# Kernel optimization log

Hardware: AMD Instinct MI355X
Metric: run time of the kernel (lower is better)

The kernel has to match this reference:

```python
import jax, jax.numpy as jnp
import numpy as np

B, T, D = 4, 2048, 256
KQ, V, H = 16, 16, 8
SCALE = float(np.sqrt(KQ))


def _lin(key, din, dout):
    k1, k2 = jax.random.split(key)
    lim = 1.0 / np.sqrt(din)
    w = jax.random.uniform(k1, (din, dout), minval=-lim, maxval=lim, dtype=jnp.float32)
    b = jax.random.uniform(k2, (dout,), minval=-lim, maxval=lim, dtype=jnp.float32)
    return w, b


def setup_inputs() -> dict:
    key = jax.random.key(0)
    ks = jax.random.split(key, 14)
    x = jax.random.normal(ks[0], (B, 3, T), dtype=jnp.float32)
    h = jax.random.normal(ks[1], (B, D, T), dtype=jnp.float32)
    q_w1, q_b1 = _lin(ks[2], D, KQ * H)
    q_w2, q_b2 = _lin(ks[3], KQ * H, KQ * H)
    k_w1, k_b1 = _lin(ks[4], D, KQ * H)
    k_w2, k_b2 = _lin(ks[5], KQ * H, KQ * H)
    v_w1, v_b1 = _lin(ks[6], D, V * H)
    v_w2, v_b2 = _lin(ks[7], V * H, V * H)
    xm_w1, xm_b1 = _lin(ks[8], V * H, V * H)
    xm_w2, xm_b2 = _lin(ks[9], V * H, H)
    ho_w, ho_b = _lin(ks[10], V * H, D)
    # GVP: Wh [v_in, dim_h], Wu [dim_h, v_out]; torch init = randn
    gvp_Wh = jax.random.normal(ks[11], (H, H), dtype=jnp.float32)
    gvp_Wu = jax.random.normal(ks[12], (H, 1), dtype=jnp.float32)
    return dict(x=x, h=h,
                q_w1=q_w1, q_b1=q_b1, q_w2=q_w2, q_b2=q_b2,
                k_w1=k_w1, k_b1=k_b1, k_w2=k_w2, k_b2=k_b2,
                v_w1=v_w1, v_b1=v_b1, v_w2=v_w2, v_b2=v_b2,
                xm_w1=xm_w1, xm_b1=xm_b1, xm_w2=xm_w2, xm_b2=xm_b2,
                ho_w=ho_w, ho_b=ho_b, gvp_Wh=gvp_Wh, gvp_Wu=gvp_Wu)


def _mlp(x, w1, b1, w2, b2):
    return jax.nn.silu(x @ w1 + b1) @ w2 + b2


def _rotate_half(t):
    # interleaved pairs (x1,x2) -> (-x2, x1), lucidrains rotary convention
    t2 = t.reshape(t.shape[:-1] + (t.shape[-1] // 2, 2))
    a, b = t2[..., 0], t2[..., 1]
    return jnp.stack((-b, a), axis=-1).reshape(t.shape)


def _rope(t):
    # t: [B, H, T, KQ]
    seq = t.shape[-2]
    inv = 1.0 / (10000.0 ** (jnp.arange(0, KQ, 2, dtype=jnp.float32) / KQ))
    f = jnp.arange(seq, dtype=jnp.float32)[:, None] * inv[None, :]   # [T, KQ/2]
    f = jnp.repeat(f, 2, axis=-1)                                    # [T, KQ]
    return t * jnp.cos(f) + _rotate_half(t) * jnp.sin(f)


def _forward(x, h,
             q_w1, q_b1, q_w2, q_b2,
             k_w1, k_b1, k_w2, k_b2,
             v_w1, v_b1, v_w2, v_b2,
             xm_w1, xm_b1, xm_w2, xm_b2,
             ho_w, ho_b, gvp_Wh, gvp_Wu):
    b, _, t = x.shape
    h_m = jnp.transpose(h, (0, 2, 1)).reshape(b * t, D)     # merge_time_dim
    q = _mlp(h_m, q_w1, q_b1, q_w2, q_b2)                   # [B*T, KQ*H]
    k = _mlp(h_m, k_w1, k_b1, k_w2, k_b2)
    v = _mlp(h_m, v_w1, v_b1, v_w2, v_b2)                   # [B*T, V*H]
    v_x = _mlp(v, xm_w1, xm_b1, xm_w2, xm_b2)               # [B*T, H]

    q = q.reshape(b, t, H, KQ).transpose(0, 2, 1, 3)        # [B,H,T,KQ]
    k = k.reshape(b, t, H, KQ).transpose(0, 2, 1, 3)
    v4 = v.reshape(b, t, H, V).transpose(0, 2, 1, 3)        # [B,H,T,V]
    v_x = v_x.reshape(b, t, H).transpose(0, 2, 1)           # [B,H,T]

    q = _rope(q)
    k = _rope(k)

    attn = jax.nn.softmax(
        jnp.einsum('bhtd,bhsd->bhts', q, k) / SCALE, axis=-1)  # [B,H,T,T]

    h_upd = jnp.einsum('bhts,bhsd->bhtd', attn, v4)         # [B,H,T,V]
    h_upd = h_upd.transpose(0, 2, 1, 3).reshape(b, t, H * V)
    h_upd = (h_upd @ ho_w + ho_b).transpose(0, 2, 1)        # [B,D,T]
    h_out = h + h_upd

    attn_w = attn * v_x[:, :, None, :]                      # weight key axis s
    gamma = attn_w.sum(axis=-1)                             # [B,H,T]
    weighted_x = jnp.einsum('bhij,bdj->bhdi', attn_w, x)    # [B,H,3,T]
    x_head = gamma[:, :, None, :] * x[:, None, :, :] - weighted_x  # [B,H,3,T]
    x_upd = x_head.transpose(0, 3, 1, 2).reshape(b * t, H, 3)      # [B*T,H,3]

    # GVP vector branch (scalar branch does not affect returned vectors)
    Vh = jnp.einsum('bvc,vh->bhc', x_upd, gvp_Wh)           # [B*T,H,3]
    Vu = jnp.einsum('bhc,hu->buc', Vh, gvp_Wu)              # [B*T,1,3]
    gate = jnp.linalg.norm(Vu, axis=-1, keepdims=True)      # [B*T,1,1]
    delta = jax.nn.sigmoid(gate) * Vu                       # [B*T,1,3]
    delta = delta[:, 0, :].reshape(b, t, 3).transpose(0, 2, 1)  # separate_time_dim -> [B,3,T]
    x_out = x + delta
    return x_out, h_out


def reference(x, h,
              q_w1, q_b1, q_w2, q_b2,
              k_w1, k_b1, k_w2, k_b2,
              v_w1, v_b1, v_w2, v_b2,
              xm_w1, xm_b1, xm_w2, xm_b2,
              ho_w, ho_b, gvp_Wh, gvp_Wu):
    return _forward(x, h,
                    q_w1, q_b1, q_w2, q_b2,
                    k_w1, k_b1, k_w2, k_b2,
                    v_w1, v_b1, v_w2, v_b2,
                    xm_w1, xm_b1, xm_w2, xm_b2,
                    ho_w, ho_b, gvp_Wh, gvp_Wu)
```

## Files before the change

kernel.cpp:

```cpp
#include <hip/hip_runtime.h>
#include <hip/hip_bf16.h>
#include <math.h>

typedef __attribute__((ext_vector_type(8))) short s16x8;
typedef __attribute__((ext_vector_type(4))) float f32x4;

__device__ __forceinline__ float silu(float a) {
    return a / (1.f + __expf(-a));
}
__device__ __forceinline__ unsigned short f2b(float f) {
    __hip_bfloat16 h = __float2bfloat16(f);
    return *reinterpret_cast<unsigned short*>(&h);
}

__global__ __launch_bounds__(256) void wprep(
    const float* __restrict__ qw1, const float* __restrict__ kw1,
    const float* __restrict__ vw1, const float* __restrict__ qw2,
    const float* __restrict__ kw2, const float* __restrict__ vw2,
    const float* __restrict__ xmw1, const float* __restrict__ xmw2,
    unsigned short* __restrict__ w1T, unsigned short* __restrict__ w2T,
    unsigned short* __restrict__ xm1T, unsigned short* __restrict__ xm2T)
{
    int idx = blockIdx.x * 256 + threadIdx.x;
    if (idx < 98304) {
        int m = idx >> 15, r = idx & 32767;
        int n = r >> 8, k = r & 255;
        const float* src = (m == 0) ? qw1 : (m == 1) ? kw1 : vw1;
        w1T[idx] = f2b(src[k * 128 + n]);
    } else if (idx < 147456) {
        int r0 = idx - 98304;
        int m = r0 >> 14, r = r0 & 16383;
        int n = r >> 7, k = r & 127;
        const float* src = (m == 0) ? qw2 : (m == 1) ? kw2 : vw2;
        w2T[r0] = f2b(src[k * 128 + n]);
    } else if (idx < 163840) {
        int r = idx - 147456;
        int n = r >> 7, k = r & 127;
        xm1T[r] = f2b(xmw1[k * 128 + n]);
    } else if (idx < 165888) {
        int r = idx - 163840;
        int n = r >> 7, k = r & 127;
        xm2T[r] = (n < 8) ? f2b(xmw2[k * 8 + n]) : (unsigned short)0;
    }
}

__global__ __launch_bounds__(256) void qkv_mfma(
    const float* __restrict__ x, const float* __restrict__ h,
    const float* __restrict__ qb1, const float* __restrict__ qb2,
    const float* __restrict__ kb1, const float* __restrict__ kb2,
    const float* __restrict__ vb1, const float* __restrict__ vb2,
    const float* __restrict__ xmb1, const float* __restrict__ xmb2,
    const unsigned short* __restrict__ w1T, const unsigned short* __restrict__ w2T,
    const unsigned short* __restrict__ xm1T, const unsigned short* __restrict__ xm2T,
    unsigned short* __restrict__ q_bf, unsigned short* __restrict__ k_bf,
    unsigned short* __restrict__ vT_bf)
{
    const int blk = blockIdx.x;
    const int b   = blk >> 7;
    const int t0  = (blk & 127) << 4;
    const int tid = threadIdx.x;
    const int nq   = tid >> 6;
    const int lane = tid & 63;
    const int m_   = lane & 15;
    const int quad = lane >> 4;

    __shared__ __align__(16) unsigned short hA[16][264];
    __shared__ __align__(16) unsigned short hidA[16][136];
    __shared__ __align__(16) unsigned short voutA[16][136];
    __shared__ float vxs[16][8];

    #pragma unroll
    for (int g = 0; g < 4; g++) {
        float4 hv = *(const float4*)(h + ((size_t)(b * 256 + tid)) * 2048
                                       + t0 + g * 4);
        hA[g * 4 + 0][tid] = f2b(hv.x);
        hA[g * 4 + 1][tid] = f2b(hv.y);
        hA[g * 4 + 2][tid] = f2b(hv.z);
        hA[g * 4 + 3][tid] = f2b(hv.w);
    }
    __syncthreads();

    auto gemm1 = [&](const unsigned short* w1m, const float* b1) {
        f32x4 acc[2] = {{0.f,0.f,0.f,0.f},{0.f,0.f,0.f,0.f}};
        #pragma unroll
        for (int kc = 0; kc < 8; kc++) {
            s16x8 af = *(const s16x8*)&hA[m_][kc * 32 + quad * 8];
            #pragma unroll
            for (int nt = 0; nt < 2; nt++) {
                const s16x8 bf = *(const s16x8*)(w1m
                    + (size_t)(nq * 32 + nt * 16 + m_) * 256 + kc * 32 + quad * 8);
                acc[nt] = __builtin_amdgcn_mfma_f32_16x16x32_bf16(
                    af, bf, acc[nt], 0, 0, 0);
            }
        }
        #pragma unroll
        for (int nt = 0; nt < 2; nt++) {
            int col = nq * 32 + nt * 16 + m_;
            float bia = b1[col];
            #pragma unroll
            for (int i = 0; i < 4; i++)
                hidA[quad * 4 + i][col] = f2b(silu(acc[nt][i] + bia));
        }
    };
    auto gemm2 = [&](const unsigned short* w2m, f32x4 acc[2]) {
        #pragma unroll
        for (int kc = 0; kc < 4; kc++) {
            s16x8 af = *(const s16x8*)&hidA[m_][kc * 32 + quad * 8];
            #pragma unroll
            for (int nt = 0; nt < 2; nt++) {
                const s16x8 bf = *(const s16x8*)(w2m
                    + (size_t)(nq * 32 + nt * 16 + m_) * 128 + kc * 32 + quad * 8);
                acc[nt] = __builtin_amdgcn_mfma_f32_16x16x32_bf16(
                    af, bf, acc[nt], 0, 0, 0);
            }
        }
    };
    auto rope_store = [&](f32x4 acc[2], const float* b2,
                          unsigned short* dst, float scale) {
        #pragma unroll
        for (int nt = 0; nt < 2; nt++) {
            int col  = nq * 32 + nt * 16 + m_;
            int head = col >> 4, dim = col & 15;
            float inv = exp2f(-(float)(dim >> 1) * 0.125f * 13.28771238f);
            float bia = b2[col];
            #pragma unroll
            for (int i = 0; i < 4; i++) {
                int t = t0 + quad * 4 + i;
                float a  = acc[nt][i] + bia;
                float pr = __shfl_xor(a, 1);
                float f  = (float)t * inv;
                float cs = cosf(f), sn = sinf(f);
                float o  = (dim & 1) ? (a * cs + pr * sn) : (a * cs - pr * sn);
                dst[((size_t)(b * 8 + head) * 2048 + t) * 16 + dim] =
                    f2b(o * scale);
            }
        }
    };

    gemm1(w1T, qb1);
    __syncthreads();
    {
        f32x4 acc[2] = {{0.f,0.f,0.f,0.f},{0.f,0.f,0.f,0.f}};
        gemm2(w2T, acc);
        rope_store(acc, qb2, q_bf, 0.25f);
    }
    __syncthreads();

    gemm1(w1T + 32768, kb1);
    __syncthreads();
    {
        f32x4 acc[2] = {{0.f,0.f,0.f,0.f},{0.f,0.f,0.f,0.f}};
        gemm2(w2T + 16384, acc);
        rope_store(acc, kb2, k_bf, 1.0f);
    }
    __syncthreads();

    gemm1(w1T + 65536, vb1);
    __syncthreads();
    {
        f32x4 acc[2] = {{0.f,0.f,0.f,0.f},{0.f,0.f,0.f,0.f}};
        gemm2(w2T + 32768, acc);
        #pragma unroll
        for (int nt = 0; nt < 2; nt++) {
            int col = nq * 32 + nt * 16 + m_;
            float bia = vb2[col];
            #pragma unroll
            for (int i = 0; i < 4; i++)
                voutA[quad * 4 + i][col] = f2b(acc[nt][i] + bia);
        }
    }
    __syncthreads();

    {
        int col = tid >> 1, tg = tid & 1;
        s16x8 pk;
        #pragma unroll
        for (int e = 0; e < 8; e++)
            pk[e] = (short)voutA[tg * 8 + e][col];
        *(s16x8*)(vT_bf + ((size_t)(b * 8 + (col >> 4)) * 32 + (col & 15)) * 2048
                        + t0 + tg * 8) = pk;
    }
    {
        f32x4 acc[2] = {{0.f,0.f,0.f,0.f},{0.f,0.f,0.f,0.f}};
        #pragma unroll
        for (int kc = 0; kc < 4; kc++) {
            s16x8 af = *(const s16x8*)&voutA[m_][kc * 32 + quad * 8];
            #pragma unroll
            for (int nt = 0; nt < 2; nt++) {
                const s16x8 bf = *(const s16x8*)(xm1T
                    + (size_t)(nq * 32 + nt * 16 + m_) * 128 + kc * 32 + quad * 8);
                acc[nt] = __builtin_amdgcn_mfma_f32_16x16x32_bf16(
                    af, bf, acc[nt], 0, 0, 0);
            }
        }
        __syncthreads();
        #pragma unroll
        for (int nt = 0; nt < 2; nt++) {
            int col = nq * 32 + nt * 16 + m_;
            float bia = xmb1[col];
            #pragma unroll
            for (int i = 0; i < 4; i++)
                hidA[quad * 4 + i][col] = f2b(silu(acc[nt][i] + bia));
        }
    }
    __syncthreads();

    if (nq == 0) {
        f32x4 a2 = {0.f, 0.f, 0.f, 0.f};
        #pragma unroll
        for (int kc = 0; kc < 4; kc++) {
            s16x8 af = *(const s16x8*)&hidA[m_][kc * 32 + quad * 8];
            const s16x8 bf = *(const s16x8*)(xm2T
                + (size_t)m_ * 128 + kc * 32 + quad * 8);
            a2 = __builtin_amdgcn_mfma_f32_16x16x32_bf16(af, bf, a2, 0, 0, 0);
        }
        if (m_ < 8) {
            float bia = xmb2[m_];
            #pragma unroll
            for (int i = 0; i < 4; i++)
                vxs[quad * 4 + i][m_] = a2[i] + bia;
        }
    }
    __syncthreads();

    #pragma unroll
    for (int r = 0; r < 2; r++) {
        int i  = tid + r * 256;
        int hh = i >> 6, c = (i >> 4) & 3, tt = i & 15;
        float val = vxs[tt][hh];
        if (c)
            val *= x[((size_t)(b * 3 + (c - 1))) * 2048 + t0 + tt];
        vT_bf[((size_t)(b * 8 + hh) * 32 + 16 + c) * 2048 + t0 + tt] = f2b(val);
    }
    if (tid < 192) {
        int hh = tid / 24, rem = tid % 24;
        int c  = 20 + (rem >> 1), tg = rem & 1;
        s16x8 z = {0,0,0,0,0,0,0,0};
        *(s16x8*)(vT_bf + ((size_t)(b * 8 + hh) * 32 + c) * 2048
                        + t0 + tg * 8) = z;
    }
}

__global__ __launch_bounds__(64) void attn_mfma(
    const unsigned short* __restrict__ q_bf,
    const unsigned short* __restrict__ k_bf,
    const unsigned short* __restrict__ vT_bf,
    float* __restrict__ opart)
{
    const int blk  = blockIdx.x;
    const int sp   = blk >> 10;
    const int bh   = (blk >> 5) & 31;
    const int qs   = (blk & 31) << 6;
    const int lane = threadIdx.x;
    const int m_   = lane & 15;
    const int quad = lane >> 4;

    __shared__ __align__(16) unsigned short Elds[4][2][16 * 72];

    const s16x8 zs = {0, 0, 0, 0, 0, 0, 0, 0};
    const f32x4 zero = {0.f, 0.f, 0.f, 0.f};

    s16x8 qfrag[4];
    #pragma unroll
    for (int qt = 0; qt < 4; qt++) {
        qfrag[qt] = zs;
        if (quad < 2)
            qfrag[qt] = *(const s16x8*)(q_bf +
                ((size_t)(bh * 2048 + qs + qt * 16 + m_) * 16 + quad * 8));
    }

    f32x4 O0[4], O1[4];
    float lsq[4];
    #pragma unroll
    for (int qt = 0; qt < 4; qt++) {
        O0[qt] = zero; O1[qt] = zero; lsq[qt] = 0.f;
    }

    const unsigned short* kb = k_bf + ((size_t)bh * 2048 + sp * 1024) * 16;
    const unsigned short* vb = vT_bf + (size_t)bh * 32 * 2048 + sp * 1024;

    for (int kt = 0; kt < 16; kt++) {
        const int k0 = kt * 64;
        const int buf = kt & 1;

        s16x8 kf[4];
        #pragma unroll
        for (int n = 0; n < 4; n++) {
            kf[n] = zs;
            if (quad < 2)
                kf[n] = *(const s16x8*)(kb +
                      ((size_t)(k0 + n * 16 + m_) * 16 + quad * 8));
        }
        s16x8 vf0[2], vf1[2];
        #pragma unroll
        for (int c = 0; c < 2; c++) {
            vf0[c] = *(const s16x8*)(vb + (size_t)m_ * 2048
                                        + k0 + c * 32 + quad * 8);
            vf1[c] = *(const s16x8*)(vb + (size_t)(16 + m_) * 2048
                                        + k0 + c * 32 + quad * 8);
        }

        #pragma unroll
        for (int qt = 0; qt < 4; qt++) {
            #pragma unroll
            for (int n = 0; n < 4; n++) {
                f32x4 E = __builtin_amdgcn_mfma_f32_16x16x32_bf16(
                    kf[n], qfrag[qt], zero, 0, 0, 0);
                float e0 = __expf(E[0]);
                float e1 = __expf(E[1]);
                float e2 = __expf(E[2]);
                float e3 = __expf(E[3]);
                lsq[qt] += e0 + e1 + e2 + e3;
                uint2 pk;
                pk.x = (unsigned)f2b(e0) | ((unsigned)f2b(e1) << 16);
                pk.y = (unsigned)f2b(e2) | ((unsigned)f2b(e3) << 16);
                *(uint2*)&Elds[qt][buf][m_ * 72 + n * 16 + quad * 4] = pk;
            }
        }
        __builtin_amdgcn_s_waitcnt(0xc07f);

        #pragma unroll
        for (int qt = 0; qt < 4; qt++) {
            #pragma unroll
            for (int c = 0; c < 2; c++) {
                s16x8 af = *(const s16x8*)
                    &Elds[qt][buf][m_ * 72 + c * 32 + quad * 8];
                O0[qt] = __builtin_amdgcn_mfma_f32_16x16x32_bf16(
                    af, vf0[c], O0[qt], 0, 0, 0);
                O1[qt] = __builtin_amdgcn_mfma_f32_16x16x32_bf16(
                    af, vf1[c], O1[qt], 0, 0, 0);
            }
        }
    }

    #pragma unroll
    for (int qt = 0; qt < 4; qt++) {
        float s = lsq[qt];
        s += __shfl_xor(s, 16);
        s += __shfl_xor(s, 32);
        float* opb = opart + ((size_t)(sp * 32 + bh) * 2048 + qs + qt * 16) * 24;
        #pragma unroll
        for (int i = 0; i < 4; i++) {
            int row = quad * 4 + i;
            float* ob = opb + row * 24;
            ob[m_] = O0[qt][i];
            if (m_ < 4) ob[16 + m_] = O1[qt][i];
        }
        if (quad == 0) opb[m_ * 24 + 20] = s;
    }
}

__global__ __launch_bounds__(256) void epi_kernel(
    const float* __restrict__ opart,
    const float* __restrict__ x, const float* __restrict__ hin,
    const float* __restrict__ how, const float* __restrict__ hob,
    const float* __restrict__ Wh, const float* __restrict__ Wu,
    float* __restrict__ out)
{
    const int blk = blockIdx.x;
    const int b  = blk >> 8;
    const int t0 = (blk & 255) << 3;
    const int tid = threadIdx.x;
    const size_t half = (size_t)32 * 2048 * 24;

    __shared__ __align__(16) float hv[128][8];
    __shared__ float gamma[8][8], wx[8][3][8];
    __shared__ float linv[8][8];
    __shared__ float weff[8];

    if (tid < 64) {
        int hh = tid >> 3, tt = tid & 7;
        size_t off = ((size_t)(b * 8 + hh) * 2048 + t0 + tt) * 24 + 20;
        linv[hh][tt] = 1.f / (opart[off] + opart[half + off]);
    } else if (tid < 72) {
        int v = tid - 64;
        float s = 0.f;
        for (int j = 0; j < 8; j++) s += Wh[v * 8 + j] * Wu[j];
        weff[v] = s;
    }
    __syncthreads();

    #pragma unroll
    for (int r = 0; r < 4; r++) {
        int i = tid + r * 256;
        int jj = i >> 3, tt = i & 7;
        size_t off = ((size_t)(b * 8 + (jj >> 4)) * 2048 + t0 + tt) * 24
                   + (jj & 15);
        hv[jj][tt] = (opart[off] + opart[half + off]) * linv[jj >> 4][tt];
    }
    {
        int hh = tid >> 5, c = (tid >> 3) & 3, tt = tid & 7;
        size_t off = ((size_t)(b * 8 + hh) * 2048 + t0 + tt) * 24 + 16 + c;
        float v = (opart[off] + opart[half + off]) * linv[hh][tt];
        if (c == 0) gamma[hh][tt] = v; else wx[hh][c - 1][tt] = v;
    }
    __syncthreads();

    f32x4 a0 = {0,0,0,0}, a1 = {0,0,0,0};
    for (int jj = 0; jj < 128; jj++) {
        float w = how[jj * 256 + tid];
        float4 v0 = *(const float4*)&hv[jj][0];
        float4 v1 = *(const float4*)&hv[jj][4];
        a0[0] += v0.x * w; a0[1] += v0.y * w; a0[2] += v0.z * w; a0[3] += v0.w * w;
        a1[0] += v1.x * w; a1[1] += v1.y * w; a1[2] += v1.z * w; a1[3] += v1.w * w;
    }
    float bias = hob[tid];
    size_t hbase = ((size_t)b * 256 + tid) * 2048 + t0;
    f32x4 accs[2] = {a0, a1};
    #pragma unroll
    for (int g = 0; g < 2; g++) {
        float4 hold = *(const float4*)(hin + hbase + g * 4);
        float4 hres;
        hres.x = hold.x + accs[g][0] + bias;
        hres.y = hold.y + accs[g][1] + bias;
        hres.z = hold.z + accs[g][2] + bias;
        hres.w = hold.w + accs[g][3] + bias;
        *(float4*)(out + 24576 + hbase + g * 4) = hres;
    }

    if (tid < 8) {
        int tt = tid;
        int t = t0 + tt;
        float Vu[3], xv[3];
        #pragma unroll
        for (int c = 0; c < 3; c++) {
            xv[c] = x[((size_t)b * 3 + c) * 2048 + t];
            float s = 0.f;
            #pragma unroll
            for (int v = 0; v < 8; v++)
                s += (gamma[v][tt] * xv[c] - wx[v][c][tt]) * weff[v];
            Vu[c] = s;
        }
        float gate = sqrtf(Vu[0]*Vu[0] + Vu[1]*Vu[1] + Vu[2]*Vu[2]);
        float sg = 1.f / (1.f + __expf(-gate));
        #pragma unroll
        for (int c = 0; c < 3; c++)
            out[((size_t)b * 3 + c) * 2048 + t] = xv[c] + sg * Vu[c];
    }
}

extern "C" void kernel_launch(void* const* d_in, const int* in_sizes, int n_in,
                              void* d_out, int out_size, void* d_ws,
                              size_t ws_size, hipStream_t stream)
{
    const float* x    = (const float*)d_in[0];
    const float* h    = (const float*)d_in[1];
    const float* qw1  = (const float*)d_in[2];
    const float* qb1  = (const float*)d_in[3];
    const float* qw2  = (const float*)d_in[4];
    const float* qb2  = (const float*)d_in[5];
    const float* kw1  = (const float*)d_in[6];
    const float* kb1  = (const float*)d_in[7];
    const float* kw2  = (const float*)d_in[8];
    const float* kb2  = (const float*)d_in[9];
    const float* vw1  = (const float*)d_in[10];
    const float* vb1  = (const float*)d_in[11];
    const float* vw2  = (const float*)d_in[12];
    const float* vb2  = (const float*)d_in[13];
    const float* xmw1 = (const float*)d_in[14];
    const float* xmb1 = (const float*)d_in[15];
    const float* xmw2 = (const float*)d_in[16];
    const float* xmb2 = (const float*)d_in[17];
    const float* how  = (const float*)d_in[18];
    const float* hob  = (const float*)d_in[19];
    const float* Wh   = (const float*)d_in[20];
    const float* Wu   = (const float*)d_in[21];
    float* out = (float*)d_out;

    unsigned short* q_bf  = (unsigned short*)d_ws;
    unsigned short* k_bf  = q_bf + (size_t)32 * 2048 * 16;
    unsigned short* vT_bf = k_bf + (size_t)32 * 2048 * 16;
    float* opart = (float*)(vT_bf + (size_t)32 * 32 * 2048);
    unsigned short* w1T  = (unsigned short*)(opart + (size_t)2 * 32 * 2048 * 24);
    unsigned short* w2T  = w1T + 98304;
    unsigned short* xm1T = w2T + 49152;
    unsigned short* xm2T = xm1T + 16384;

    wprep<<<648, 256, 0, stream>>>(qw1, kw1, vw1, qw2, kw2, vw2, xmw1, xmw2,
                                   w1T, w2T, xm1T, xm2T);
    qkv_mfma<<<512, 256, 0, stream>>>(
        x, h, qb1, qb2, kb1, kb2, vb1, vb2, xmb1, xmb2,
        w1T, w2T, xm1T, xm2T, q_bf, k_bf, vT_bf);
    attn_mfma<<<2048, 64, 0, stream>>>(q_bf, k_bf, vT_bf, opart);
    epi_kernel<<<1024, 256, 0, stream>>>(opart, x, h, how, hob, Wh, Wu, out);
}
```

Before: 187.2 us.

## Use bf16 MFMA for epilogue output projection and batch QKV GEMMs

The epilogue's scalar fp32 loop over the 128x256 output projection is replaced with bf16 MFMA tiles over 16 timesteps per block. The projection weight is transposed and converted to bf16 in the prep kernel, and the grid is halved. In the QKV kernel, the three first-layer GEMMs are interleaved in one loop into separate shared buffers, which cuts barriers and exposes more MFMA parallelism. The cost is bf16 rounding of the attention output before the projection, plus higher register and LDS use.

```diff
diff --git a/kernel.cpp b/kernel.cpp
--- a/kernel.cpp
+++ b/kernel.cpp
@@ -18,8 +18,10 @@
     const float* __restrict__ vw1, const float* __restrict__ qw2,
     const float* __restrict__ kw2, const float* __restrict__ vw2,
     const float* __restrict__ xmw1, const float* __restrict__ xmw2,
+    const float* __restrict__ how,
     unsigned short* __restrict__ w1T, unsigned short* __restrict__ w2T,
-    unsigned short* __restrict__ xm1T, unsigned short* __restrict__ xm2T)
+    unsigned short* __restrict__ xm1T, unsigned short* __restrict__ xm2T,
+    unsigned short* __restrict__ howT)
 {
     int idx = blockIdx.x * 256 + threadIdx.x;
     if (idx < 98304) {
@@ -41,6 +43,10 @@
         int r = idx - 163840;
         int n = r >> 7, k = r & 127;
         xm2T[r] = (n < 8) ? f2b(xmw2[k * 8 + n]) : (unsigned short)0;
+    } else if (idx < 198656) {
+        int r = idx - 165888;
+        int n = r >> 7, k = r & 127;
+        howT[r] = f2b(how[k * 256 + n]);
     }
 }
 
@@ -65,7 +71,9 @@
     const int quad = lane >> 4;
 
     __shared__ __align__(16) unsigned short hA[16][264];
-    __shared__ __align__(16) unsigned short hidA[16][136];
+    __shared__ __align__(16) unsigned short hidQ[16][136];
+    __shared__ __align__(16) unsigned short hidK[16][136];
+    __shared__ __align__(16) unsigned short hidV[16][136];
     __shared__ __align__(16) unsigned short voutA[16][136];
     __shared__ float vxs[16][8];
 
@@ -80,32 +88,44 @@
     }
     __syncthreads();
 
-    auto gemm1 = [&](const unsigned short* w1m, const float* b1) {
-        f32x4 acc[2] = {{0.f,0.f,0.f,0.f},{0.f,0.f,0.f,0.f}};
+    const f32x4 zero = {0.f, 0.f, 0.f, 0.f};
+
+    {
+        f32x4 aQ[2] = {zero, zero}, aK[2] = {zero, zero}, aV[2] = {zero, zero};
         #pragma unroll
         for (int kc = 0; kc < 8; kc++) {
             s16x8 af = *(const s16x8*)&hA[m_][kc * 32 + quad * 8];
             #pragma unroll
             for (int nt = 0; nt < 2; nt++) {
-                const s16x8 bf = *(const s16x8*)(w1m
-                    + (size_t)(nq * 32 + nt * 16 + m_) * 256 + kc * 32 + quad * 8);
-                acc[nt] = __builtin_amdgcn_mfma_f32_16x16x32_bf16(
-                    af, bf, acc[nt], 0, 0, 0);
+                size_t woff = (size_t)(nq * 32 + nt * 16 + m_) * 256
+                            + kc * 32 + quad * 8;
+                aQ[nt] = __builtin_amdgcn_mfma_f32_16x16x32_bf16(
+                    af, *(const s16x8*)(w1T + woff), aQ[nt], 0, 0, 0);
+                aK[nt] = __builtin_amdgcn_mfma_f32_16x16x32_bf16(
+                    af, *(const s16x8*)(w1T + 32768 + woff), aK[nt], 0, 0, 0);
+                aV[nt] = __builtin_amdgcn_mfma_f32_16x16x32_bf16(
+                    af, *(const s16x8*)(w1T + 65536 + woff), aV[nt], 0, 0, 0);
             }
         }
         #pragma unroll
         for (int nt = 0; nt < 2; nt++) {
             int col = nq * 32 + nt * 16 + m_;
-            float bia = b1[col];
-            #pragma unroll
-            for (int i = 0; i < 4; i++)
-                hidA[quad * 4 + i][col] = f2b(silu(acc[nt][i] + bia));
-        }
-    };
-    auto gemm2 = [&](const unsigned short* w2m, f32x4 acc[2]) {
+            float bq = qb1[col], bk = kb1[col], bv = vb1[col];
+            #pragma unroll
+            for (int i = 0; i < 4; i++) {
+                hidQ[quad * 4 + i][col] = f2b(silu(aQ[nt][i] + bq));
+                hidK[quad * 4 + i][col] = f2b(silu(aK[nt][i] + bk));
+                hidV[quad * 4 + i][col] = f2b(silu(aV[nt][i] + bv));
+            }
+        }
+    }
+    __syncthreads();
+
+    auto gemm2 = [&](const unsigned short* w2m,
+                     unsigned short (*hid)[136], f32x4 acc[2]) {
         #pragma unroll
         for (int kc = 0; kc < 4; kc++) {
-            s16x8 af = *(const s16x8*)&hidA[m_][kc * 32 + quad * 8];
+            s16x8 af = *(const s16x8*)&hid[m_][kc * 32 + quad * 8];
             #pragma unroll
             for (int nt = 0; nt < 2; nt++) {
                 const s16x8 bf = *(const s16x8*)(w2m
@@ -137,36 +157,20 @@
         }
     };
 
-    gemm1(w1T, qb1);
-    __syncthreads();
     {
-        f32x4 acc[2] = {{0.f,0.f,0.f,0.f},{0.f,0.f,0.f,0.f}};
-        gemm2(w2T, acc);
-        rope_store(acc, qb2, q_bf, 0.25f);
-    }
-    __syncthreads();
-
-    gemm1(w1T + 32768, kb1);
-    __syncthreads();
-    {
-        f32x4 acc[2] = {{0.f,0.f,0.f,0.f},{0.f,0.f,0.f,0.f}};
-        gemm2(w2T + 16384, acc);
-        rope_store(acc, kb2, k_bf, 1.0f);
-    }
-    __syncthreads();
-
-    gemm1(w1T + 65536, vb1);
-    __syncthreads();
-    {
-        f32x4 acc[2] = {{0.f,0.f,0.f,0.f},{0.f,0.f,0.f,0.f}};
-        gemm2(w2T + 32768, acc);
+        f32x4 aQ[2] = {zero, zero}, aK[2] = {zero, zero}, aV[2] = {zero, zero};
+        gemm2(w2T,         hidQ, aQ);
+        gemm2(w2T + 16384, hidK, aK);
+        gemm2(w2T + 32768, hidV, aV);
+        rope_store(aQ, qb2, q_bf, 0.25f);
+        rope_store(aK, kb2, k_bf, 1.0f);
         #pragma unroll
         for (int nt = 0; nt < 2; nt++) {
             int col = nq * 32 + nt * 16 + m_;
             float bia = vb2[col];
             #pragma unroll
             for (int i = 0; i < 4; i++)
-                voutA[quad * 4 + i][col] = f2b(acc[nt][i] + bia);
+                voutA[quad * 4 + i][col] = f2b(aV[nt][i] + bia);
         }
     }
     __syncthreads();
@@ -181,7 +185,7 @@
                         + t0 + tg * 8) = pk;
     }
     {
-        f32x4 acc[2] = {{0.f,0.f,0.f,0.f},{0.f,0.f,0.f,0.f}};
+        f32x4 acc[2] = {zero, zero};
         #pragma unroll
         for (int kc = 0; kc < 4; kc++) {
             s16x8 af = *(const s16x8*)&voutA[m_][kc * 32 + quad * 8];
@@ -193,23 +197,22 @@
                     af, bf, acc[nt], 0, 0, 0);
             }
         }
-        __syncthreads();
         #pragma unroll
         for (int nt = 0; nt < 2; nt++) {
             int col = nq * 32 + nt * 16 + m_;
             float bia = xmb1[col];
             #pragma unroll
             for (int i = 0; i < 4; i++)
-                hidA[quad * 4 + i][col] = f2b(silu(acc[nt][i] + bia));
+                hidQ[quad * 4 + i][col] = f2b(silu(acc[nt][i] + bia));
         }
     }
     __syncthreads();
 
     if (nq == 0) {
-        f32x4 a2 = {0.f, 0.f, 0.f, 0.f};
+        f32x4 a2 = zero;
         #pragma unroll
         for (int kc = 0; kc < 4; kc++) {
-            s16x8 af = *(const s16x8*)&hidA[m_][kc * 32 + quad * 8];
+            s16x8 af = *(const s16x8*)&hidQ[m_][kc * 32 + quad * 8];
             const s16x8 bf = *(const s16x8*)(xm2T
                 + (size_t)m_ * 128 + kc * 32 + quad * 8);
             a2 = __builtin_amdgcn_mfma_f32_16x16x32_bf16(af, bf, a2, 0, 0, 0);
@@ -351,29 +354,33 @@
 }
 
 __global__ __launch_bounds__(256) void epi_kernel(
-    const float* __restrict__ opart,
+    const float* __restrict__ opart, const unsigned short* __restrict__ howT,
     const float* __restrict__ x, const float* __restrict__ hin,
-    const float* __restrict__ how, const float* __restrict__ hob,
+    const float* __restrict__ hob,
     const float* __restrict__ Wh, const float* __restrict__ Wu,
     float* __restrict__ out)
 {
     const int blk = blockIdx.x;
-    const int b  = blk >> 8;
-    const int t0 = (blk & 255) << 3;
+    const int b  = blk >> 7;
+    const int t0 = (blk & 127) << 4;
     const int tid = threadIdx.x;
+    const int nq   = tid >> 6;
+    const int lane = tid & 63;
+    const int m_   = lane & 15;
+    const int quad = lane >> 4;
     const size_t half = (size_t)32 * 2048 * 24;
 
-    __shared__ __align__(16) float hv[128][8];
-    __shared__ float gamma[8][8], wx[8][3][8];
-    __shared__ float linv[8][8];
+    __shared__ __align__(16) unsigned short hvA[16][136];
+    __shared__ float linv[8][16];
+    __shared__ float gamma[8][16], wx[8][3][16];
     __shared__ float weff[8];
 
-    if (tid < 64) {
-        int hh = tid >> 3, tt = tid & 7;
+    if (tid < 128) {
+        int hh = tid >> 4, tt = tid & 15;
         size_t off = ((size_t)(b * 8 + hh) * 2048 + t0 + tt) * 24 + 20;
         linv[hh][tt] = 1.f / (opart[off] + opart[half + off]);
-    } else if (tid < 72) {
-        int v = tid - 64;
+    } else if (tid < 136) {
+        int v = tid - 128;
         float s = 0.f;
         for (int j = 0; j < 8; j++) s += Wh[v * 8 + j] * Wu[j];
         weff[v] = s;
@@ -381,44 +388,48 @@
     __syncthreads();
 
     #pragma unroll
-    for (int r = 0; r < 4; r++) {
+    for (int r = 0; r < 8; r++) {
         int i = tid + r * 256;
-        int jj = i >> 3, tt = i & 7;
+        int jj = i >> 4, tt = i & 15;
         size_t off = ((size_t)(b * 8 + (jj >> 4)) * 2048 + t0 + tt) * 24
                    + (jj & 15);
-        hv[jj][tt] = (opart[off] + opart[half + off]) * linv[jj >> 4][tt];
-    }
-    {
-        int hh = tid >> 5, c = (tid >> 3) & 3, tt = tid & 7;
+        hvA[tt][jj] =
+            f2b((opart[off] + opart[half + off]) * linv[jj >> 4][tt]);
+    }
+    #pragma unroll
+    for (int r = 0; r < 2; r++) {
+        int i = tid + r * 256;
+        int hh = i >> 6, c = (i >> 4) & 3, tt = i & 15;
         size_t off = ((size_t)(b * 8 + hh) * 2048 + t0 + tt) * 24 + 16 + c;
         float v = (opart[off] + opart[half + off]) * linv[hh][tt];
         if (c == 0) gamma[hh][tt] = v; else wx[hh][c - 1][tt] = v;
     }
     __syncthreads();
 
-    f32x4 a0 = {0,0,0,0}, a1 = {0,0,0,0};
-    for (int jj = 0; jj < 128; jj++) {
-        float w = how[jj * 256 + tid];
-        float4 v0 = *(const float4*)&hv[jj][0];
-        float4 v1 = *(const float4*)&hv[jj][4];
-        a0[0] += v0.x * w; a0[1] += v0.y * w; a0[2] += v0.z * w; a0[3] += v0.w * w;
-        a1[0] += v1.x * w; a1[1] += v1.y * w; a1[2] += v1.z * w; a1[3] += v1.w * w;
-    }
-    float bias = hob[tid];
-    size_t hbase = ((size_t)b * 256 + tid) * 2048 + t0;
-    f32x4 accs[2] = {a0, a1};
-    #pragma unroll
-    for (int g = 0; g < 2; g++) {
-        float4 hold = *(const float4*)(hin + hbase + g * 4);
+    const f32x4 zero = {0.f, 0.f, 0.f, 0.f};
+    #pragma unroll
+    for (int nt = 0; nt < 4; nt++) {
+        int col = nq * 64 + nt * 16 + m_;
+        f32x4 acc = zero;
+        #pragma unroll
+        for (int kc = 0; kc < 4; kc++) {
+            s16x8 af = *(const s16x8*)&hvA[m_][kc * 32 + quad * 8];
+            const s16x8 bf = *(const s16x8*)(howT
+                + (size_t)col * 128 + kc * 32 + quad * 8);
+            acc = __builtin_amdgcn_mfma_f32_16x16x32_bf16(af, bf, acc, 0, 0, 0);
+        }
+        float bia = hob[col];
+        size_t base = ((size_t)b * 256 + col) * 2048 + t0 + quad * 4;
+        float4 hold = *(const float4*)(hin + base);
         float4 hres;
-        hres.x = hold.x + accs[g][0] + bias;
-        hres.y = hold.y + accs[g][1] + bias;
-        hres.z = hold.z + accs[g][2] + bias;
-        hres.w = hold.w + accs[g][3] + bias;
-        *(float4*)(out + 24576 + hbase + g * 4) = hres;
-    }
-
-    if (tid < 8) {
+        hres.x = hold.x + acc[0] + bia;
+        hres.y = hold.y + acc[1] + bia;
+        hres.z = hold.z + acc[2] + bia;
+        hres.w = hold.w + acc[3] + bia;
+        *(float4*)(out + 24576 + base) = hres;
+    }
+
+    if (tid < 16) {
         int tt = tid;
         int t = t0 + tt;
         float Vu[3], xv[3];
@@ -475,12 +486,13 @@
     unsigned short* w2T  = w1T + 98304;
     unsigned short* xm1T = w2T + 49152;
     unsigned short* xm2T = xm1T + 16384;
-
-    wprep<<<648, 256, 0, stream>>>(qw1, kw1, vw1, qw2, kw2, vw2, xmw1, xmw2,
-                                   w1T, w2T, xm1T, xm2T);
+    unsigned short* howT = xm2T + 2048;
+
+    wprep<<<776, 256, 0, stream>>>(qw1, kw1, vw1, qw2, kw2, vw2, xmw1, xmw2,
+                                   how, w1T, w2T, xm1T, xm2T, howT);
     qkv_mfma<<<512, 256, 0, stream>>>(
         x, h, qb1, qb2, kb1, kb2, vb1, vb2, xmb1, xmb2,
         w1T, w2T, xm1T, xm2T, q_bf, k_bf, vT_bf);
     attn_mfma<<<2048, 64, 0, stream>>>(q_bf, k_bf, vT_bf, opart);
-    epi_kernel<<<1024, 256, 0, stream>>>(opart, x, h, how, hob, Wh, Wu, out);
-}
+    epi_kernel<<<512, 256, 0, stream>>>(opart, howT, x, h, hob, Wh, Wu, out);
+}
```

New measurement: 183.9 us. About the same (-1.7%).
